# Performance work log

Measured on AMD Instinct MI355X. Metric: run time of the kernel, lower is better.

## Reference

```python
import jax, jax.numpy as jnp
import numpy as np

NUM_EXPERTS = 64


def setup_inputs() -> dict:
    key = jax.random.key(0)
    k1, k2 = jax.random.split(key)
    x = jax.random.normal(k1, (4, 4096, 2048), dtype=jnp.float32)
    # nn.Linear default init scale ~ 1/sqrt(dim); exact init irrelevant for correctness
    gate_w = jax.random.normal(k2, (NUM_EXPERTS, 2048), dtype=jnp.float32) * (1.0 / np.sqrt(2048.0))
    expert_bias = jnp.zeros((NUM_EXPERTS,), dtype=jnp.float32)
    return {"x": x, "gate_w": gate_w, "expert_bias": expert_bias, "top_k": 8}


def reference(x, gate_w, expert_bias, top_k):
    # x: [B, S, D]; gate_w: [E, D]; expert_bias: [E]
    B, S, D = x.shape
    x_flat = x.reshape(-1, D)                                  # [T, D], T = B*S
    logits = jnp.einsum('td,ed->te', x_flat, gate_w) + expert_bias  # [T, E]
    top_k_logits, top_k_indices = jax.lax.top_k(logits, top_k)      # [T, K]
    top_k_weights = jax.nn.softmax(top_k_logits, axis=-1)           # [T, K]
    # training-mode load counting (scatter_add over expert ids)
    expert_counts = jax.ops.segment_sum(
        jnp.ones((B * S * top_k,), dtype=jnp.float32),
        top_k_indices.reshape(-1),
        num_segments=NUM_EXPERTS,
    )                                                               # [E]
    return top_k_indices, top_k_weights, expert_counts
```

## Files before the change

### kernel.cpp

```cpp
#include <hip/hip_runtime.h>
#include <math.h>

#define T_TOKENS 16384
#define D_DIM    2048
#define E_EXP    64
#define TOPK     8


#define TT   64
#define KC   32
#define XT   68
#define GT   68

__global__ __launch_bounds__(256, 4) void moe_logits_kernel(
    const float* __restrict__ x, const float* __restrict__ gw,
    float* __restrict__ part, float* __restrict__ counts_zero, int ns)
{
  __shared__ float xl[KC * XT];
  __shared__ float gl[KC * GT];

  const int tid  = threadIdx.x;
  const int tg   = tid & 15;
  const int eg   = tid >> 4;
  const int ks   = blockIdx.y;
  const int tok0 = blockIdx.x * TT;
  const int ksz  = D_DIM / ns;
  const int k0   = ks * ksz;
  const int nchunk = ksz / KC;

  if (blockIdx.x == 0 && ks == 0 && tid < E_EXP) counts_zero[tid] = 0.0f;

  const int srow = tid >> 2;
  const int sq   = tid & 3;

  float4 acc[4];
  #pragma unroll
  for (int j = 0; j < 4; ++j) acc[j] = make_float4(0.f, 0.f, 0.f, 0.f);

  #pragma unroll 1
  for (int c = 0; c < nchunk; ++c) {
    const int kc0 = k0 + c * KC;

    #pragma unroll
    for (int p = 0; p < 2; ++p) {
      const int kk = (sq + 4 * p) * 4;
      float4 v = *(const float4*)&x[(size_t)(tok0 + srow) * D_DIM + kc0 + kk];
      xl[(kk + 0) * XT + srow] = v.x;
      xl[(kk + 1) * XT + srow] = v.y;
      xl[(kk + 2) * XT + srow] = v.z;
      xl[(kk + 3) * XT + srow] = v.w;
    }
    #pragma unroll
    for (int p = 0; p < 2; ++p) {
      const int kk = (sq + 4 * p) * 4;
      float4 v = *(const float4*)&gw[(size_t)srow * D_DIM + kc0 + kk];
      gl[(kk + 0) * GT + srow] = v.x;
      gl[(kk + 1) * GT + srow] = v.y;
      gl[(kk + 2) * GT + srow] = v.z;
      gl[(kk + 3) * GT + srow] = v.w;
    }
    __syncthreads();

    #pragma unroll
    for (int k = 0; k < KC; ++k) {
      float4 xv = *(const float4*)&xl[k * XT + tg * 4];
      float4 gv = *(const float4*)&gl[k * GT + eg * 4];
      acc[0].x = fmaf(xv.x, gv.x, acc[0].x); acc[0].y = fmaf(xv.x, gv.y, acc[0].y);
      acc[0].z = fmaf(xv.x, gv.z, acc[0].z); acc[0].w = fmaf(xv.x, gv.w, acc[0].w);
      acc[1].x = fmaf(xv.y, gv.x, acc[1].x); acc[1].y = fmaf(xv.y, gv.y, acc[1].y);
      acc[1].z = fmaf(xv.y, gv.z, acc[1].z); acc[1].w = fmaf(xv.y, gv.w, acc[1].w);
      acc[2].x = fmaf(xv.z, gv.x, acc[2].x); acc[2].y = fmaf(xv.z, gv.y, acc[2].y);
      acc[2].z = fmaf(xv.z, gv.z, acc[2].z); acc[2].w = fmaf(xv.z, gv.w, acc[2].w);
      acc[3].x = fmaf(xv.w, gv.x, acc[3].x); acc[3].y = fmaf(xv.w, gv.y, acc[3].y);
      acc[3].z = fmaf(xv.w, gv.z, acc[3].z); acc[3].w = fmaf(xv.w, gv.w, acc[3].w);
    }
    __syncthreads();
  }

  #pragma unroll
  for (int j = 0; j < 4; ++j) {
    const size_t t = (size_t)tok0 + tg * 4 + j;
    *(float4*)&part[((size_t)ks * T_TOKENS + t) * E_EXP + eg * 4] = acc[j];
  }
}

__global__ __launch_bounds__(64) void topk_kernel(
    const float* __restrict__ part, const float* __restrict__ bias,
    float* __restrict__ out, int ns)
{
  __shared__ unsigned hist[E_EXP];
  const int tid = threadIdx.x;
  const int t = blockIdx.x * 64 + tid;
  hist[tid] = 0;
  __syncthreads();

  float l[E_EXP];
  #pragma unroll
  for (int j = 0; j < E_EXP / 4; ++j) {
    float4 b = *(const float4*)&bias[j * 4];
    l[4*j] = b.x; l[4*j+1] = b.y; l[4*j+2] = b.z; l[4*j+3] = b.w;
  }
  for (int ks = 0; ks < ns; ++ks) {
    const float4* p = (const float4*)&part[((size_t)ks * T_TOKENS + t) * E_EXP];
    #pragma unroll
    for (int j = 0; j < E_EXP / 4; ++j) {
      float4 v = p[j];
      l[4*j] += v.x; l[4*j+1] += v.y; l[4*j+2] += v.z; l[4*j+3] += v.w;
    }
  }

  float tv[TOPK]; int tix[TOPK];
  unsigned long long used = 0ull;
  #pragma unroll
  for (int k = 0; k < TOPK; ++k) {
    float best = -INFINITY; int bi = 0;
    #pragma unroll
    for (int j = 0; j < E_EXP; ++j) {
      bool ok = (((used >> j) & 1ull) == 0ull) && (l[j] > best);
      best = ok ? l[j] : best;
      bi   = ok ? j : bi;
    }
    tv[k] = best; tix[k] = bi;
    used |= (1ull << bi);
  }

  float m = tv[0], s = 0.0f, w[TOPK];
  #pragma unroll
  for (int k = 0; k < TOPK; ++k) { w[k] = expf(tv[k] - m); s += w[k]; }
  float inv = 1.0f / s;

  #pragma unroll
  for (int k = 0; k < TOPK; ++k) {
    out[(size_t)t * TOPK + k] = (float)tix[k];
    out[(size_t)T_TOKENS * TOPK + (size_t)t * TOPK + k] = w[k] * inv;
  }

  #pragma unroll
  for (int k = 0; k < TOPK; ++k) atomicAdd(&hist[tix[k]], 1u);
  __syncthreads();
  atomicAdd(&out[2 * (size_t)T_TOKENS * TOPK + tid], (float)hist[tid]);
}

extern "C" void kernel_launch(void* const* d_in, const int* in_sizes, int n_in,
                              void* d_out, int out_size, void* d_ws, size_t ws_size,
                              hipStream_t stream) {
  const float* x    = (const float*)d_in[0];
  const float* gw   = (const float*)d_in[1];
  const float* bias = (const float*)d_in[2];
  float* out  = (float*)d_out;
  float* part = (float*)d_ws;

  const size_t slice_bytes = (size_t)T_TOKENS * E_EXP * sizeof(float);
  int ns = 1;
  if (ws_size >= 4 * slice_bytes)      ns = 4;
  else if (ws_size >= 2 * slice_bytes) ns = 2;

  moe_logits_kernel<<<dim3(T_TOKENS / TT, ns), dim3(256), 0, stream>>>(
      x, gw, part, out + 2 * (size_t)T_TOKENS * TOPK, ns);
  topk_kernel<<<dim3(T_TOKENS / 64), dim3(64), 0, stream>>>(part, bias, out, ns);
}
```

Measured before the change: 236.3 us.

## Enlarge logits GEMM register tile to 8x8 and allow deeper K-split

Each thread of the logits kernel now computes an 8-token by 8-expert register tile instead of 4x4. The block is 128 threads covering 128 tokens, with padded LDS offsets so the wider float4 reads avoid bank conflicts. This halves the LDS reads per FMA, which targets the LDS-bound inner loop. The host also picks an 8-way K split when the workspace is large enough, keeping enough blocks in flight at the cost of more partial-sum traffic for the top-k kernel. The 64 accumulators per thread raise register pressure.

```diff
diff --git a/kernel.cpp b/kernel.cpp
--- a/kernel.cpp
+++ b/kernel.cpp
@@ -7,12 +7,12 @@
 #define TOPK     8
 
 
-#define TT   64
+#define TT   128
 #define KC   32
-#define XT   68
+#define XT   132
 #define GT   68
 
-__global__ __launch_bounds__(256, 4) void moe_logits_kernel(
+__global__ __launch_bounds__(128, 2) void moe_logits_kernel(
     const float* __restrict__ x, const float* __restrict__ gw,
     float* __restrict__ part, float* __restrict__ counts_zero, int ns)
 {
@@ -30,57 +30,70 @@
 
   if (blockIdx.x == 0 && ks == 0 && tid < E_EXP) counts_zero[tid] = 0.0f;
 
-  const int srow = tid >> 2;
-  const int sq   = tid & 3;
+  const int xbase = tg * 8 + 4 * (tg >> 3);
 
-  float4 acc[4];
+  float4 acc[16];
   #pragma unroll
-  for (int j = 0; j < 4; ++j) acc[j] = make_float4(0.f, 0.f, 0.f, 0.f);
+  for (int j = 0; j < 16; ++j) acc[j] = make_float4(0.f, 0.f, 0.f, 0.f);
 
   #pragma unroll 1
   for (int c = 0; c < nchunk; ++c) {
     const int kc0 = k0 + c * KC;
 
     #pragma unroll
-    for (int p = 0; p < 2; ++p) {
-      const int kk = (sq + 4 * p) * 4;
-      float4 v = *(const float4*)&x[(size_t)(tok0 + srow) * D_DIM + kc0 + kk];
-      xl[(kk + 0) * XT + srow] = v.x;
-      xl[(kk + 1) * XT + srow] = v.y;
-      xl[(kk + 2) * XT + srow] = v.z;
-      xl[(kk + 3) * XT + srow] = v.w;
+    for (int p = 0; p < 8; ++p) {
+      const int flat = p * 128 + tid;
+      const int row  = flat >> 3;
+      const int c4   = flat & 7;
+      float4 v = *(const float4*)&x[(size_t)(tok0 + row) * D_DIM + kc0 + c4 * 4];
+      const int pos = row + 4 * (row >> 6);
+      xl[(c4 * 4 + 0) * XT + pos] = v.x;
+      xl[(c4 * 4 + 1) * XT + pos] = v.y;
+      xl[(c4 * 4 + 2) * XT + pos] = v.z;
+      xl[(c4 * 4 + 3) * XT + pos] = v.w;
     }
     #pragma unroll
-    for (int p = 0; p < 2; ++p) {
-      const int kk = (sq + 4 * p) * 4;
-      float4 v = *(const float4*)&gw[(size_t)srow * D_DIM + kc0 + kk];
-      gl[(kk + 0) * GT + srow] = v.x;
-      gl[(kk + 1) * GT + srow] = v.y;
-      gl[(kk + 2) * GT + srow] = v.z;
-      gl[(kk + 3) * GT + srow] = v.w;
+    for (int p = 0; p < 4; ++p) {
+      const int flat = p * 128 + tid;
+      const int erow = flat >> 3;
+      const int c4   = flat & 7;
+      float4 v = *(const float4*)&gw[(size_t)erow * D_DIM + kc0 + c4 * 4];
+      gl[(c4 * 4 + 0) * GT + erow] = v.x;
+      gl[(c4 * 4 + 1) * GT + erow] = v.y;
+      gl[(c4 * 4 + 2) * GT + erow] = v.z;
+      gl[(c4 * 4 + 3) * GT + erow] = v.w;
     }
     __syncthreads();
 
     #pragma unroll
     for (int k = 0; k < KC; ++k) {
-      float4 xv = *(const float4*)&xl[k * XT + tg * 4];
-      float4 gv = *(const float4*)&gl[k * GT + eg * 4];
-      acc[0].x = fmaf(xv.x, gv.x, acc[0].x); acc[0].y = fmaf(xv.x, gv.y, acc[0].y);
-      acc[0].z = fmaf(xv.x, gv.z, acc[0].z); acc[0].w = fmaf(xv.x, gv.w, acc[0].w);
-      acc[1].x = fmaf(xv.y, gv.x, acc[1].x); acc[1].y = fmaf(xv.y, gv.y, acc[1].y);
-      acc[1].z = fmaf(xv.y, gv.z, acc[1].z); acc[1].w = fmaf(xv.y, gv.w, acc[1].w);
-      acc[2].x = fmaf(xv.z, gv.x, acc[2].x); acc[2].y = fmaf(xv.z, gv.y, acc[2].y);
-      acc[2].z = fmaf(xv.z, gv.z, acc[2].z); acc[2].w = fmaf(xv.z, gv.w, acc[2].w);
-      acc[3].x = fmaf(xv.w, gv.x, acc[3].x); acc[3].y = fmaf(xv.w, gv.y, acc[3].y);
-      acc[3].z = fmaf(xv.w, gv.z, acc[3].z); acc[3].w = fmaf(xv.w, gv.w, acc[3].w);
+      float4 xv0 = *(const float4*)&xl[k * XT + xbase];
+      float4 xv1 = *(const float4*)&xl[k * XT + xbase + 4];
+      float4 gv0 = *(const float4*)&gl[k * GT + eg * 8];
+      float4 gv1 = *(const float4*)&gl[k * GT + eg * 8 + 4];
+      const float xs[8] = {xv0.x, xv0.y, xv0.z, xv0.w, xv1.x, xv1.y, xv1.z, xv1.w};
+      #pragma unroll
+      for (int j = 0; j < 8; ++j) {
+        const float xj = xs[j];
+        acc[j*2+0].x = fmaf(xj, gv0.x, acc[j*2+0].x);
+        acc[j*2+0].y = fmaf(xj, gv0.y, acc[j*2+0].y);
+        acc[j*2+0].z = fmaf(xj, gv0.z, acc[j*2+0].z);
+        acc[j*2+0].w = fmaf(xj, gv0.w, acc[j*2+0].w);
+        acc[j*2+1].x = fmaf(xj, gv1.x, acc[j*2+1].x);
+        acc[j*2+1].y = fmaf(xj, gv1.y, acc[j*2+1].y);
+        acc[j*2+1].z = fmaf(xj, gv1.z, acc[j*2+1].z);
+        acc[j*2+1].w = fmaf(xj, gv1.w, acc[j*2+1].w);
+      }
     }
     __syncthreads();
   }
 
   #pragma unroll
-  for (int j = 0; j < 4; ++j) {
-    const size_t t = (size_t)tok0 + tg * 4 + j;
-    *(float4*)&part[((size_t)ks * T_TOKENS + t) * E_EXP + eg * 4] = acc[j];
+  for (int j = 0; j < 8; ++j) {
+    const size_t t = (size_t)tok0 + tg * 8 + j;
+    float* pp = &part[((size_t)ks * T_TOKENS + t) * E_EXP + eg * 8];
+    *(float4*)&pp[0] = acc[j*2+0];
+    *(float4*)&pp[4] = acc[j*2+1];
   }
 }
 
@@ -152,10 +165,11 @@
 
   const size_t slice_bytes = (size_t)T_TOKENS * E_EXP * sizeof(float);
   int ns = 1;
-  if (ws_size >= 4 * slice_bytes)      ns = 4;
+  if (ws_size >= 8 * slice_bytes)      ns = 8;
+  else if (ws_size >= 4 * slice_bytes) ns = 4;
   else if (ws_size >= 2 * slice_bytes) ns = 2;
 
-  moe_logits_kernel<<<dim3(T_TOKENS / TT, ns), dim3(256), 0, stream>>>(
+  moe_logits_kernel<<<dim3(T_TOKENS / TT, ns), dim3(128), 0, stream>>>(
       x, gw, part, out + 2 * (size_t)T_TOKENS * TOPK, ns);
   topk_kernel<<<dim3(T_TOKENS / 64), dim3(64), 0, stream>>>(part, bias, out, ns);
 }
```

Measured after the change: 238.5 us. Within noise of the previous version (+0.9%).
